# Kernel tuning notes

Hardware: AMD Instinct MI355X
Metric: run time of the kernel (lower is better)

The kernel has to match this reference:

```python
import jax, jax.numpy as jnp
import numpy as np

FP8_MAX = 448.0  # max finite value of float8_e4m3fn
EPS = 1e-12


def _quantize_fp8(t):
    """Per-tensor dynamic fp8 quantization: returns (fp8_tensor, scale) where
    dequant = fp8.astype(f32) / scale, matching the torch module's math."""
    t32 = t.astype(jnp.float32)
    amax = jnp.maximum(jnp.max(jnp.abs(t32)), EPS)
    scale = FP8_MAX / amax
    t_fp8 = jnp.clip(t32 * scale, -FP8_MAX, FP8_MAX).astype(jnp.float8_e4m3fn)
    return t_fp8, scale


def setup_inputs() -> dict:
    key = jax.random.key(0)
    kx, kw, kb = jax.random.split(key, 3)
    M, K, N = 4096, 4096, 4096  # tokens, in_features, out_features
    x = jax.random.normal(kx, (M, K), dtype=jnp.float16)
    weight = jax.random.normal(kw, (N, K), dtype=jnp.float16)
    bias = jax.random.normal(kb, (N,), dtype=jnp.float16)
    return {"x": x, "weight": weight, "bias": bias}


def reference(x, weight, bias):
    # weight pre-quantization (quantize_weight)
    w_fp8, w_scale = _quantize_fp8(weight)
    # dynamic activation quantization
    x_fp8, x_scale = _quantize_fp8(x)
    # scaled_mm: (x_fp8 @ w_fp8.T) * scale_a * scale_b, out fp16
    acc = jnp.einsum(
        "mk,nk->mn",
        x_fp8.astype(jnp.float32),
        w_fp8.astype(jnp.float32),
        preferred_element_type=jnp.float32,
    )
    out = (acc * (1.0 / x_scale) * (1.0 / w_scale)).astype(jnp.float16)
    out = out + bias
    return out
```

## Files before the change

kernel.cpp:

```cpp
#include <hip/hip_runtime.h>
#include <hip/hip_fp16.h>

typedef __bf16 bf16x8 __attribute__((ext_vector_type(8)));
typedef float f32x4 __attribute__((ext_vector_type(4)));
typedef int i32x8 __attribute__((ext_vector_type(8)));
typedef unsigned short ushort8 __attribute__((ext_vector_type(8)));

#define TM 128
#define TN 128
#define TK 128
#define FP8MAX 448.0f
#define SCALE_ONE 0x7F7F7F7FU

__global__ __launch_bounds__(256)
void amax_stage1(const float* __restrict__ in, unsigned n4,
                 float* __restrict__ blockmax) {
    __shared__ float wmax[4];
    unsigned tid = blockIdx.x * 256 + threadIdx.x;
    unsigned stride = gridDim.x * 256;
    float m = 0.f;
    for (unsigned i = tid; i < n4; i += stride) {
        float4 v = *(const float4*)(in + (size_t)i * 4);
        m = fmaxf(m, fmaxf(fmaxf(fabsf(v.x), fabsf(v.y)), fmaxf(fabsf(v.z), fabsf(v.w))));
    }
#pragma unroll
    for (int off = 32; off > 0; off >>= 1)
        m = fmaxf(m, __shfl_down(m, off));
    if ((threadIdx.x & 63) == 0) wmax[threadIdx.x >> 6] = m;
    __syncthreads();
    if (threadIdx.x == 0)
        blockmax[blockIdx.x] = fmaxf(fmaxf(wmax[0], wmax[1]), fmaxf(wmax[2], wmax[3]));
}

__global__ __launch_bounds__(256)
void amax_stage2(const float* __restrict__ bm, int n, float* __restrict__ outv) {
    __shared__ float wmax[4];
    const float* p = bm + (size_t)blockIdx.x * n;
    float m = 0.f;
    for (int i = threadIdx.x; i < n; i += 256) m = fmaxf(m, p[i]);
#pragma unroll
    for (int off = 32; off > 0; off >>= 1)
        m = fmaxf(m, __shfl_down(m, off));
    if ((threadIdx.x & 63) == 0) wmax[threadIdx.x >> 6] = m;
    __syncthreads();
    if (threadIdx.x == 0)
        outv[blockIdx.x] = fmaxf(fmaxf(wmax[0], wmax[1]), fmaxf(wmax[2], wmax[3]));
}

__global__ __launch_bounds__(256)
void quant_kernel(const float* __restrict__ in, uint2* __restrict__ out,
                  const float* __restrict__ amax_p, unsigned n8) {
    float amax = fmaxf(*amax_p, 1e-12f);
    float scale = FP8MAX / amax;
    unsigned tid = blockIdx.x * 256 + threadIdx.x;
    unsigned stride = gridDim.x * 256;
    for (unsigned i = tid; i < n8; i += stride) {
        float4 lo = *(const float4*)(in + (size_t)i * 8);
        float4 hi = *(const float4*)(in + (size_t)i * 8 + 4);
        float f[8] = {lo.x, lo.y, lo.z, lo.w, hi.x, hi.y, hi.z, hi.w};
#pragma unroll
        for (int j = 0; j < 8; ++j)
            f[j] = fminf(fmaxf(f[j] * scale, -FP8MAX), FP8MAX);
        unsigned w0 = __builtin_amdgcn_cvt_pk_fp8_f32(f[0], f[1], 0u, false);
        w0 = __builtin_amdgcn_cvt_pk_fp8_f32(f[2], f[3], w0, true);
        unsigned w1 = __builtin_amdgcn_cvt_pk_fp8_f32(f[4], f[5], 0u, false);
        w1 = __builtin_amdgcn_cvt_pk_fp8_f32(f[6], f[7], w1, true);
        out[i] = make_uint2(w0, w1);
    }
}

__device__ inline void gl2lds16(const void* g, void* l) {
    __builtin_amdgcn_global_load_lds(
        (const __attribute__((address_space(1))) unsigned int*)g,
        (__attribute__((address_space(3))) unsigned int*)l, 16, 0, 0);
}

__device__ inline void epilogue(f32x4 acc[4][4], const float* bias, float* C,
                                float rs, int row0, int col0, int wr, int wc,
                                int lane, int N) {
    int crow0 = row0 + wr * 64;
    int ccol0 = col0 + wc * 64 + (lane & 15);
    int rsub = (lane >> 4) * 4;
#pragma unroll
    for (int n = 0; n < 4; ++n) {
        int col = ccol0 + n * 16;
        float bv = bias[col];
#pragma unroll
        for (int m = 0; m < 4; ++m) {
#pragma unroll
            for (int j = 0; j < 4; ++j) {
                int row = crow0 + m * 16 + rsub + j;
                float t = __half2float(__float2half_rn(acc[m][n][j] * rs));
                C[(size_t)row * N + col] = __half2float(__float2half_rn(t + bv));
            }
        }
    }
}

__global__ __launch_bounds__(256)
void gemm_kernel(const unsigned char* __restrict__ A,
                 const unsigned char* __restrict__ B,
                 const float* __restrict__ bias,
                 float* __restrict__ C,
                 const float* __restrict__ amax2,
                 int M, int N, int K) {
    __shared__ uint4 As4[TM * TK / 16];
    __shared__ uint4 Bs4[TN * TK / 16];
    char* As = (char*)As4;
    char* Bs = (char*)Bs4;

    int tid = threadIdx.x;
    int lane = tid & 63;
    int wave = tid >> 6;
    int row0 = blockIdx.y * TM;
    int col0 = blockIdx.x * TN;
    int wr = wave >> 1, wc = wave & 1;

    f32x4 acc[4][4];
#pragma unroll
    for (int m = 0; m < 4; ++m)
#pragma unroll
        for (int n = 0; n < 4; ++n)
            acc[m][n] = (f32x4){0.f, 0.f, 0.f, 0.f};

    int frow = lane & 15;
    int fk = (lane >> 4) * 32;

    for (int kt = 0; kt < K; kt += TK) {
#pragma unroll
        for (int i = 0; i < 4; ++i) {
            int s = i * 256 + tid;
            int r = s >> 3, c = s & 7;
            gl2lds16(A + (size_t)(row0 + r) * K + kt + c * 16,
                     As + (i * 256 + wave * 64) * 16);
            gl2lds16(B + (size_t)(col0 + r) * K + kt + c * 16,
                     Bs + (i * 256 + wave * 64) * 16);
        }
        __syncthreads();

        union { i32x8 v; uint4 q[2]; } af[4], bf[4];
#pragma unroll
        for (int m = 0; m < 4; ++m) {
            const char* p = As + (wr * 64 + m * 16 + frow) * TK + fk;
            af[m].q[0] = *(const uint4*)p;
            af[m].q[1] = *(const uint4*)(p + 16);
        }
#pragma unroll
        for (int n = 0; n < 4; ++n) {
            const char* p = Bs + (wc * 64 + n * 16 + frow) * TK + fk;
            bf[n].q[0] = *(const uint4*)p;
            bf[n].q[1] = *(const uint4*)(p + 16);
        }
#pragma unroll
        for (int m = 0; m < 4; ++m)
#pragma unroll
            for (int n = 0; n < 4; ++n)
                acc[m][n] = __builtin_amdgcn_mfma_scale_f32_16x16x128_f8f6f4(
                    af[m].v, bf[n].v, acc[m][n],
                    0, 0,
                    0, SCALE_ONE,
                    0, SCALE_ONE);
        __syncthreads();
    }

    float ax = fmaxf(amax2[0], 1e-12f);
    float aw = fmaxf(amax2[1], 1e-12f);
    float rs = (ax / FP8MAX) * (aw / FP8MAX);
    epilogue(acc, bias, C, rs, row0, col0, wr, wc, lane, N);
}

__device__ inline ushort8 quant8f_bf16(float4 lo, float4 hi, float scale) {
    float f[8] = {lo.x, lo.y, lo.z, lo.w, hi.x, hi.y, hi.z, hi.w};
    ushort8 r;
#pragma unroll
    for (int j = 0; j < 4; ++j) {
        float f0 = fminf(fmaxf(f[2 * j] * scale, -FP8MAX), FP8MAX);
        float f1 = fminf(fmaxf(f[2 * j + 1] * scale, -FP8MAX), FP8MAX);
        unsigned pk = __builtin_amdgcn_cvt_pk_fp8_f32(f0, f1, 0u, false);
        float d0 = __builtin_amdgcn_cvt_f32_fp8(pk, 0);
        float d1 = __builtin_amdgcn_cvt_f32_fp8(pk, 1);
        r[2 * j]     = (unsigned short)(__float_as_uint(d0) >> 16);
        r[2 * j + 1] = (unsigned short)(__float_as_uint(d1) >> 16);
    }
    return r;
}

__global__ __launch_bounds__(256)
void gemm_fused(const float* __restrict__ X, const float* __restrict__ W,
                const float* __restrict__ bias, float* __restrict__ C,
                const float* __restrict__ amax2, int M, int N, int K) {
    __shared__ ushort8 As8[TM * 64 / 8];
    __shared__ ushort8 Bs8[TN * 64 / 8];
    char* As = (char*)As8;
    char* Bs = (char*)Bs8;

    float ax = fmaxf(amax2[0], 1e-12f);
    float aw = fmaxf(amax2[1], 1e-12f);
    float sx = FP8MAX / ax, sw = FP8MAX / aw;

    int tid = threadIdx.x;
    int lane = tid & 63;
    int wave = tid >> 6;
    int row0 = blockIdx.y * TM;
    int col0 = blockIdx.x * TN;
    int wr = wave >> 1, wc = wave & 1;

    f32x4 acc[4][4];
#pragma unroll
    for (int m = 0; m < 4; ++m)
#pragma unroll
        for (int n = 0; n < 4; ++n)
            acc[m][n] = (f32x4){0.f, 0.f, 0.f, 0.f};

    int frow = lane & 15;
    int fksub = (lane >> 4) * 16;

    for (int kt = 0; kt < K; kt += 64) {
#pragma unroll
        for (int i = 0; i < 4; ++i) {
            int s = i * 256 + tid;
            int r = s >> 3, c = s & 7;
            const float* pa = X + (size_t)(row0 + r) * K + kt + c * 8;
            const float* pb = W + (size_t)(col0 + r) * K + kt + c * 8;
            float4 a0 = *(const float4*)pa, a1 = *(const float4*)(pa + 4);
            float4 b0 = *(const float4*)pb, b1 = *(const float4*)(pb + 4);
            *(ushort8*)(As + s * 16) = quant8f_bf16(a0, a1, sx);
            *(ushort8*)(Bs + s * 16) = quant8f_bf16(b0, b1, sw);
        }
        __syncthreads();

#pragma unroll
        for (int kk = 0; kk < 2; ++kk) {
            bf16x8 af[4], bfr[4];
#pragma unroll
            for (int m = 0; m < 4; ++m)
                af[m] = *(const bf16x8*)(As + (wr * 64 + m * 16 + frow) * 128 + kk * 64 + fksub);
#pragma unroll
            for (int n = 0; n < 4; ++n)
                bfr[n] = *(const bf16x8*)(Bs + (wc * 64 + n * 16 + frow) * 128 + kk * 64 + fksub);
#pragma unroll
            for (int m = 0; m < 4; ++m)
#pragma unroll
                for (int n = 0; n < 4; ++n)
                    acc[m][n] = __builtin_amdgcn_mfma_f32_16x16x32_bf16(af[m], bfr[n], acc[m][n], 0, 0, 0);
        }
        __syncthreads();
    }

    float rs = (ax / FP8MAX) * (aw / FP8MAX);
    epilogue(acc, bias, C, rs, row0, col0, wr, wc, lane, N);
}

extern "C" void kernel_launch(void* const* d_in, const int* in_sizes, int n_in,
                              void* d_out, int out_size, void* d_ws, size_t ws_size,
                              hipStream_t stream) {
    const float* x = (const float*)d_in[0];
    const float* w = (const float*)d_in[1];
    const float* bias = (const float*)d_in[2];
    float* out = (float*)d_out;

    int N = in_sizes[2];
    int K = in_sizes[1] / N;
    int M = in_sizes[0] / K;

    float* bmx = (float*)d_ws;
    float* bmw = bmx + 1024;
    float* amax2 = bmx + 2048;
    unsigned char* xq = (unsigned char*)d_ws + 16384;
    unsigned char* wq = xq + (size_t)M * K;

    unsigned n4x = (unsigned)((size_t)M * K / 4);
    unsigned n4w = (unsigned)((size_t)N * K / 4);

    amax_stage1<<<1024, 256, 0, stream>>>(x, n4x, bmx);
    amax_stage1<<<1024, 256, 0, stream>>>(w, n4w, bmw);
    amax_stage2<<<2, 256, 0, stream>>>(bmx, 1024, amax2);

    dim3 grid(N / TN, M / TM);
    size_t needA = (size_t)M * K + (size_t)N * K + 16384;

    if (ws_size >= needA) {
        quant_kernel<<<2048, 256, 0, stream>>>(x, (uint2*)xq, amax2 + 0,
                                               (unsigned)((size_t)M * K / 8));
        quant_kernel<<<2048, 256, 0, stream>>>(w, (uint2*)wq, amax2 + 1,
                                               (unsigned)((size_t)N * K / 8));
        gemm_kernel<<<grid, 256, 0, stream>>>(xq, wq, bias, out, amax2, M, N, K);
    } else {
        gemm_fused<<<grid, 256, 0, stream>>>(x, w, bias, out, amax2, M, N, K);
    }
}
```

Baseline: 149.3 us.

## Triple-buffer fp8 GEMM with swizzled LDS, larger tiles, and merged prep kernels

The fp8 GEMM moves to 256x128 tiles with 512 threads. It uses a three-slot LDS ring loaded asynchronously two tiles ahead, with manual vmcnt waits and barriers in place of the per-tile syncthreads. LDS rows are XOR-swizzled to avoid bank conflicts, and setprio is raised around the MFMA block. The x and w amax and quantize passes are each merged into a single launch to cut launch overhead. In exchange it uses 144KB of dynamic LDS, needs the more complex wait-count logic to be exactly right, and has fewer blocks in the grid.

```diff
diff --git a/kernel.cpp b/kernel.cpp
--- a/kernel.cpp
+++ b/kernel.cpp
@@ -6,20 +6,26 @@
 typedef int i32x8 __attribute__((ext_vector_type(8)));
 typedef unsigned short ushort8 __attribute__((ext_vector_type(8)));
 
-#define TM 128
-#define TN 128
-#define TK 128
+#define BM 256
+#define BN 128
+#define BK 128
 #define FP8MAX 448.0f
 #define SCALE_ONE 0x7F7F7F7FU
+#define A_BYTES (BM * BK)
+#define B_BYTES (BN * BK)
+#define SLOT_BYTES (A_BYTES + B_BYTES)
 
 __global__ __launch_bounds__(256)
-void amax_stage1(const float* __restrict__ in, unsigned n4,
-                 float* __restrict__ blockmax) {
+void amax_stage1(const float* __restrict__ x, unsigned n4x,
+                 const float* __restrict__ w, unsigned n4w,
+                 float* __restrict__ bm) {
     __shared__ float wmax[4];
-    unsigned tid = blockIdx.x * 256 + threadIdx.x;
-    unsigned stride = gridDim.x * 256;
+    bool isw = blockIdx.x >= 1024;
+    const float* in = isw ? w : x;
+    unsigned n4 = isw ? n4w : n4x;
+    unsigned tid = (blockIdx.x & 1023) * 256 + threadIdx.x;
     float m = 0.f;
-    for (unsigned i = tid; i < n4; i += stride) {
+    for (unsigned i = tid; i < n4; i += 1024 * 256) {
         float4 v = *(const float4*)(in + (size_t)i * 4);
         m = fmaxf(m, fmaxf(fmaxf(fabsf(v.x), fabsf(v.y)), fmaxf(fabsf(v.z), fabsf(v.w))));
     }
@@ -29,15 +35,15 @@
     if ((threadIdx.x & 63) == 0) wmax[threadIdx.x >> 6] = m;
     __syncthreads();
     if (threadIdx.x == 0)
-        blockmax[blockIdx.x] = fmaxf(fmaxf(wmax[0], wmax[1]), fmaxf(wmax[2], wmax[3]));
+        bm[blockIdx.x] = fmaxf(fmaxf(wmax[0], wmax[1]), fmaxf(wmax[2], wmax[3]));
 }
 
 __global__ __launch_bounds__(256)
-void amax_stage2(const float* __restrict__ bm, int n, float* __restrict__ outv) {
+void amax_stage2(const float* __restrict__ bm, float* __restrict__ outv) {
     __shared__ float wmax[4];
-    const float* p = bm + (size_t)blockIdx.x * n;
+    const float* p = bm + (size_t)blockIdx.x * 1024;
     float m = 0.f;
-    for (int i = threadIdx.x; i < n; i += 256) m = fmaxf(m, p[i]);
+    for (int i = threadIdx.x; i < 1024; i += 256) m = fmaxf(m, p[i]);
 #pragma unroll
     for (int off = 32; off > 0; off >>= 1)
         m = fmaxf(m, __shfl_down(m, off));
@@ -48,13 +54,18 @@
 }
 
 __global__ __launch_bounds__(256)
-void quant_kernel(const float* __restrict__ in, uint2* __restrict__ out,
-                  const float* __restrict__ amax_p, unsigned n8) {
-    float amax = fmaxf(*amax_p, 1e-12f);
+void quant_kernel(const float* __restrict__ x, unsigned n8x,
+                  const float* __restrict__ w, unsigned n8w,
+                  unsigned char* __restrict__ xq, unsigned char* __restrict__ wq,
+                  const float* __restrict__ amax2) {
+    bool isw = blockIdx.x >= 2048;
+    const float* in = isw ? w : x;
+    uint2* out = (uint2*)(isw ? wq : xq);
+    unsigned n8 = isw ? n8w : n8x;
+    float amax = fmaxf(amax2[isw ? 1 : 0], 1e-12f);
     float scale = FP8MAX / amax;
-    unsigned tid = blockIdx.x * 256 + threadIdx.x;
-    unsigned stride = gridDim.x * 256;
-    for (unsigned i = tid; i < n8; i += stride) {
+    unsigned tid = (blockIdx.x & 2047) * 256 + threadIdx.x;
+    for (unsigned i = tid; i < n8; i += 2048 * 256) {
         float4 lo = *(const float4*)(in + (size_t)i * 8);
         float4 hi = *(const float4*)(in + (size_t)i * 8 + 4);
         float f[8] = {lo.x, lo.y, lo.z, lo.w, hi.x, hi.y, hi.z, hi.w};
@@ -75,46 +86,22 @@
         (__attribute__((address_space(3))) unsigned int*)l, 16, 0, 0);
 }
 
-__device__ inline void epilogue(f32x4 acc[4][4], const float* bias, float* C,
-                                float rs, int row0, int col0, int wr, int wc,
-                                int lane, int N) {
-    int crow0 = row0 + wr * 64;
-    int ccol0 = col0 + wc * 64 + (lane & 15);
-    int rsub = (lane >> 4) * 4;
-#pragma unroll
-    for (int n = 0; n < 4; ++n) {
-        int col = ccol0 + n * 16;
-        float bv = bias[col];
-#pragma unroll
-        for (int m = 0; m < 4; ++m) {
-#pragma unroll
-            for (int j = 0; j < 4; ++j) {
-                int row = crow0 + m * 16 + rsub + j;
-                float t = __half2float(__float2half_rn(acc[m][n][j] * rs));
-                C[(size_t)row * N + col] = __half2float(__float2half_rn(t + bv));
-            }
-        }
-    }
-}
-
-__global__ __launch_bounds__(256)
+__global__ __launch_bounds__(512, 2)
 void gemm_kernel(const unsigned char* __restrict__ A,
                  const unsigned char* __restrict__ B,
                  const float* __restrict__ bias,
                  float* __restrict__ C,
                  const float* __restrict__ amax2,
                  int M, int N, int K) {
-    __shared__ uint4 As4[TM * TK / 16];
-    __shared__ uint4 Bs4[TN * TK / 16];
-    char* As = (char*)As4;
-    char* Bs = (char*)Bs4;
+    extern __shared__ char LDS[];
 
     int tid = threadIdx.x;
     int lane = tid & 63;
     int wave = tid >> 6;
-    int row0 = blockIdx.y * TM;
-    int col0 = blockIdx.x * TN;
-    int wr = wave >> 1, wc = wave & 1;
+    int wr = wave >> 1;
+    int wc = wave & 1;
+    int row0 = blockIdx.y * BM;
+    int col0 = blockIdx.x * BN;
 
     f32x4 acc[4][4];
 #pragma unroll
@@ -124,49 +111,111 @@
             acc[m][n] = (f32x4){0.f, 0.f, 0.f, 0.f};
 
     int frow = lane & 15;
-    int fk = (lane >> 4) * 32;
-
-    for (int kt = 0; kt < K; kt += TK) {
+    int g32 = (lane >> 4) * 32;
+
+    const int NT = K >> 7;
+
+    auto STAGE = [&](int t, int si) {
+        char* slot = LDS + si * SLOT_BYTES;
 #pragma unroll
         for (int i = 0; i < 4; ++i) {
-            int s = i * 256 + tid;
+            int s = i * 512 + tid;
             int r = s >> 3, c = s & 7;
-            gl2lds16(A + (size_t)(row0 + r) * K + kt + c * 16,
-                     As + (i * 256 + wave * 64) * 16);
-            gl2lds16(B + (size_t)(col0 + r) * K + kt + c * 16,
-                     Bs + (i * 256 + wave * 64) * 16);
-        }
-        __syncthreads();
-
-        union { i32x8 v; uint4 q[2]; } af[4], bf[4];
+            gl2lds16(A + (size_t)(row0 + r) * K + t * BK + ((c ^ (r & 7)) << 4),
+                     slot + s * 16);
+        }
+#pragma unroll
+        for (int i = 0; i < 2; ++i) {
+            int s = i * 512 + tid;
+            int r = s >> 3, c = s & 7;
+            gl2lds16(B + (size_t)(col0 + r) * K + t * BK + ((c ^ (r & 7)) << 4),
+                     slot + A_BYTES + s * 16);
+        }
+    };
+
+    STAGE(0, 0);
+    if (NT > 1) {
+        STAGE(1, 1);
+        __builtin_amdgcn_sched_barrier(0);
+        asm volatile("s_waitcnt vmcnt(6)" ::: "memory");
+    } else {
+        __builtin_amdgcn_sched_barrier(0);
+        asm volatile("s_waitcnt vmcnt(0)" ::: "memory");
+    }
+    __builtin_amdgcn_s_barrier();
+    __builtin_amdgcn_sched_barrier(0);
+
+    int cur = 0;
+    for (int t = 0; t < NT; ++t) {
+        if (t + 2 < NT) {
+            int stg = (cur == 0) ? 2 : cur - 1;
+            STAGE(t + 2, stg);
+        }
+
+        char* As = LDS + cur * SLOT_BYTES;
+        char* Bs = As + A_BYTES;
+        union U { i32x8 v; uint4 q[2]; };
+        U af[4], bf[4];
 #pragma unroll
         for (int m = 0; m < 4; ++m) {
-            const char* p = As + (wr * 64 + m * 16 + frow) * TK + fk;
-            af[m].q[0] = *(const uint4*)p;
-            af[m].q[1] = *(const uint4*)(p + 16);
+            int row = wr * 64 + m * 16 + frow;
+            int c0 = g32 ^ ((row & 7) << 4);
+            const char* p = As + row * 128;
+            af[m].q[0] = *(const uint4*)(p + c0);
+            af[m].q[1] = *(const uint4*)(p + (c0 ^ 16));
         }
 #pragma unroll
         for (int n = 0; n < 4; ++n) {
-            const char* p = Bs + (wc * 64 + n * 16 + frow) * TK + fk;
-            bf[n].q[0] = *(const uint4*)p;
-            bf[n].q[1] = *(const uint4*)(p + 16);
-        }
+            int row = wc * 64 + n * 16 + frow;
+            int c0 = g32 ^ ((row & 7) << 4);
+            const char* p = Bs + row * 128;
+            bf[n].q[0] = *(const uint4*)(p + c0);
+            bf[n].q[1] = *(const uint4*)(p + (c0 ^ 16));
+        }
+
+        __builtin_amdgcn_s_setprio(1);
 #pragma unroll
         for (int m = 0; m < 4; ++m)
 #pragma unroll
             for (int n = 0; n < 4; ++n)
                 acc[m][n] = __builtin_amdgcn_mfma_scale_f32_16x16x128_f8f6f4(
                     af[m].v, bf[n].v, acc[m][n],
-                    0, 0,
-                    0, SCALE_ONE,
-                    0, SCALE_ONE);
-        __syncthreads();
+                    0, 0, 0, SCALE_ONE, 0, SCALE_ONE);
+        __builtin_amdgcn_s_setprio(0);
+
+        if (t + 1 < NT) {
+            __builtin_amdgcn_sched_barrier(0);
+            if (t + 2 < NT)
+                asm volatile("s_waitcnt vmcnt(6)" ::: "memory");
+            else
+                asm volatile("s_waitcnt vmcnt(0)" ::: "memory");
+            __builtin_amdgcn_s_barrier();
+            __builtin_amdgcn_sched_barrier(0);
+        }
+        cur = (cur == 2) ? 0 : cur + 1;
     }
 
     float ax = fmaxf(amax2[0], 1e-12f);
     float aw = fmaxf(amax2[1], 1e-12f);
     float rs = (ax / FP8MAX) * (aw / FP8MAX);
-    epilogue(acc, bias, C, rs, row0, col0, wr, wc, lane, N);
+
+    int crow0 = row0 + wr * 64;
+    int ccol0 = col0 + wc * 64 + frow;
+    int rsub = (lane >> 4) * 4;
+#pragma unroll
+    for (int n = 0; n < 4; ++n) {
+        int col = ccol0 + n * 16;
+        float bv = bias[col];
+#pragma unroll
+        for (int m = 0; m < 4; ++m) {
+#pragma unroll
+            for (int j = 0; j < 4; ++j) {
+                int row = crow0 + m * 16 + rsub + j;
+                float tcl = __half2float(__float2half_rn(acc[m][n][j] * rs));
+                C[(size_t)row * N + col] = __half2float(__float2half_rn(tcl + bv));
+            }
+        }
+    }
 }
 
 __device__ inline ushort8 quant8f_bf16(float4 lo, float4 hi, float scale) {
@@ -189,8 +238,8 @@
 void gemm_fused(const float* __restrict__ X, const float* __restrict__ W,
                 const float* __restrict__ bias, float* __restrict__ C,
                 const float* __restrict__ amax2, int M, int N, int K) {
-    __shared__ ushort8 As8[TM * 64 / 8];
-    __shared__ ushort8 Bs8[TN * 64 / 8];
+    __shared__ ushort8 As8[128 * 64 / 8];
+    __shared__ ushort8 Bs8[128 * 64 / 8];
     char* As = (char*)As8;
     char* Bs = (char*)Bs8;
 
@@ -201,8 +250,8 @@
     int tid = threadIdx.x;
     int lane = tid & 63;
     int wave = tid >> 6;
-    int row0 = blockIdx.y * TM;
-    int col0 = blockIdx.x * TN;
+    int row0 = blockIdx.y * 128;
+    int col0 = blockIdx.x * 128;
     int wr = wave >> 1, wc = wave & 1;
 
     f32x4 acc[4][4];
@@ -248,7 +297,23 @@
     }
 
     float rs = (ax / FP8MAX) * (aw / FP8MAX);
-    epilogue(acc, bias, C, rs, row0, col0, wr, wc, lane, N);
+    int crow0 = row0 + wr * 64;
+    int ccol0 = col0 + wc * 64 + frow;
+    int rsub = (lane >> 4) * 4;
+#pragma unroll
+    for (int n = 0; n < 4; ++n) {
+        int col = ccol0 + n * 16;
+        float bv = bias[col];
+#pragma unroll
+        for (int m = 0; m < 4; ++m) {
+#pragma unroll
+            for (int j = 0; j < 4; ++j) {
+                int row = crow0 + m * 16 + rsub + j;
+                float t = __half2float(__float2half_rn(acc[m][n][j] * rs));
+                C[(size_t)row * N + col] = __half2float(__float2half_rn(t + bv));
+            }
+        }
+    }
 }
 
 extern "C" void kernel_launch(void* const* d_in, const int* in_sizes, int n_in,
@@ -263,29 +328,27 @@
     int K = in_sizes[1] / N;
     int M = in_sizes[0] / K;
 
-    float* bmx = (float*)d_ws;
-    float* bmw = bmx + 1024;
-    float* amax2 = bmx + 2048;
+    float* bm = (float*)d_ws;
+    float* amax2 = bm + 2048;
     unsigned char* xq = (unsigned char*)d_ws + 16384;
     unsigned char* wq = xq + (size_t)M * K;
 
     unsigned n4x = (unsigned)((size_t)M * K / 4);
     unsigned n4w = (unsigned)((size_t)N * K / 4);
 
-    amax_stage1<<<1024, 256, 0, stream>>>(x, n4x, bmx);
-    amax_stage1<<<1024, 256, 0, stream>>>(w, n4w, bmw);
-    amax_stage2<<<2, 256, 0, stream>>>(bmx, 1024, amax2);
-
-    dim3 grid(N / TN, M / TM);
+    amax_stage1<<<2048, 256, 0, stream>>>(x, n4x, w, n4w, bm);
+    amax_stage2<<<2, 256, 0, stream>>>(bm, amax2);
+
     size_t needA = (size_t)M * K + (size_t)N * K + 16384;
 
-    if (ws_size >= needA) {
-        quant_kernel<<<2048, 256, 0, stream>>>(x, (uint2*)xq, amax2 + 0,
-                                               (unsigned)((size_t)M * K / 8));
-        quant_kernel<<<2048, 256, 0, stream>>>(w, (uint2*)wq, amax2 + 1,
-                                               (unsigned)((size_t)N * K / 8));
-        gemm_kernel<<<grid, 256, 0, stream>>>(xq, wq, bias, out, amax2, M, N, K);
+    if (ws_size >= needA && (M % BM) == 0 && (N % BN) == 0 && (K % BK) == 0 && K / BK >= 2) {
+        quant_kernel<<<4096, 256, 0, stream>>>(x, (unsigned)((size_t)M * K / 8),
+                                               w, (unsigned)((size_t)N * K / 8),
+                                               xq, wq, amax2);
+        dim3 grid(N / BN, M / BM);
+        gemm_kernel<<<grid, 512, 3 * SLOT_BYTES, stream>>>(xq, wq, bias, out, amax2, M, N, K);
     } else {
+        dim3 grid(N / 128, M / 128);
         gemm_fused<<<grid, 256, 0, stream>>>(x, w, bias, out, amax2, M, N, K);
     }
 }
```

Result: faster. 145.4 us (-2.6%).
